# Performance work log

Hardware: AMD Instinct MI355X
Metric: run time of the kernel (lower is better)

The kernel has to match this reference:

```python
import jax, jax.numpy as jnp
import numpy as np

N_NODES = 50000
N_EDGES = 600000
HIDDEN = 128
HEADS = 4
HEAD_DIM = HIDDEN // HEADS
RBF = 40


def setup_inputs() -> dict:
    key = jax.random.key(0)
    ks = jax.random.split(key, 16)
    def lin(k, fan_in, fan_out):
        return jax.random.normal(k, (fan_in, fan_out), jnp.float32) / np.sqrt(fan_in)
    return {
        "x": jax.random.normal(ks[0], (N_NODES, HIDDEN), jnp.float32),
        "edge_index": jax.random.randint(ks[1], (2, N_EDGES), 0, N_NODES, jnp.int32),
        "edge_attr_rbf": jax.random.normal(ks[2], (N_EDGES, RBF), jnp.float32),
        "is_defect": jax.random.randint(ks[3], (N_NODES,), 0, 2, jnp.int32),
        "Wq": lin(ks[4], HIDDEN, HIDDEN), "bq": jnp.zeros((HIDDEN,), jnp.float32),
        "Wk": lin(ks[5], HIDDEN, HIDDEN), "bk": jnp.zeros((HIDDEN,), jnp.float32),
        "Wv": lin(ks[6], HIDDEN, HIDDEN), "bv": jnp.zeros((HIDDEN,), jnp.float32),
        "Wo": lin(ks[7], HIDDEN, HIDDEN), "bo": jnp.zeros((HIDDEN,), jnp.float32),
        "Wg1": lin(ks[8], RBF, HIDDEN), "bg1": jnp.zeros((HIDDEN,), jnp.float32),
        "Wg2": lin(ks[9], HIDDEN, HEADS), "bg2": jnp.zeros((HEADS,), jnp.float32),
        "defect_bias": jax.random.normal(ks[10], (HEADS, 4), jnp.float32),
    }


def reference(x, edge_index, edge_attr_rbf, is_defect,
              Wq, bq, Wk, bk, Wv, bv, Wo, bo, Wg1, bg1, Wg2, bg2, defect_bias):
    N = x.shape[0]
    Q = (x @ Wq + bq).reshape(N, HEADS, HEAD_DIM)
    K = (x @ Wk + bk).reshape(N, HEADS, HEAD_DIM)
    V = (x @ Wv + bv).reshape(N, HEADS, HEAD_DIM)
    src, dst = edge_index[0], edge_index[1]
    # per-edge attention scores [E, H]
    score = (Q[src] * K[dst]).sum(-1) / np.sqrt(HEAD_DIM)
    geo_bias = jax.nn.silu(edge_attr_rbf @ Wg1 + bg1) @ Wg2 + bg2  # [E, H]
    defect_code = is_defect[src] * 2 + is_defect[dst]  # [E] in {0,1,2,3}
    score = score + geo_bias + defect_bias[:, defect_code].T
    # segment softmax over edges grouped by dst
    smax = jax.ops.segment_max(score, dst, num_segments=N)  # [N, H]
    e = jnp.exp(score - smax[dst])
    denom = jax.ops.segment_sum(e, dst, num_segments=N)  # [N, H]
    alpha = e / denom[dst]
    msg = V[src] * alpha[..., None]  # [E, H, Hd]
    out = jax.ops.segment_sum(msg, dst, num_segments=N).reshape(N, HIDDEN)
    return out @ Wo + bo
```

## Files before the change

kernel.cpp:

```cpp
#include <hip/hip_runtime.h>
#include <math.h>

#define NN 50000
#define NE 600000
#define HID 128
#define NH 4
#define HD 32
#define NRBF 40
#define SCALE 0.17677669529663687f

typedef __attribute__((ext_vector_type(8))) __bf16 bf16x8;
typedef __attribute__((ext_vector_type(4))) __bf16 bf16x4;
typedef __attribute__((ext_vector_type(4))) float f32x4;

#define MFMA16(a, b, c) __builtin_amdgcn_mfma_f32_16x16x32_bf16(a, b, c, 0, 0, 0)

__device__ __forceinline__ void split2(float v, __bf16& h, __bf16& l) {
  h = (__bf16)v;
  l = (__bf16)(v - (float)h);
}

__global__ void k_prepw(const float* __restrict__ W, __bf16* __restrict__ hi,
                        __bf16* __restrict__ lo, int NKS, int KREAL) {
  int slot = blockIdx.x * 256 + threadIdx.x;
  int total = 8 * NKS * 4 * 16;
  if (slot >= total) return;
  int n = slot & 15, kg = (slot >> 4) & 3;
  int tt = slot >> 6;
  int ks = tt % NKS, nt = tt / NKS;
  bf16x8 h8, l8;
#pragma unroll
  for (int j = 0; j < 8; ++j) {
    int k = ks * 32 + kg * 8 + j;
    float v = (k < KREAL) ? W[k * 128 + nt * 16 + n] : 0.f;
    __bf16 h, l;
    split2(v, h, l);
    h8[j] = h;
    l8[j] = l;
  }
  *(bf16x8*)&hi[slot * 8] = h8;
  *(bf16x8*)&lo[slot * 8] = l8;
}

__global__ __launch_bounds__(256) void k_qkv3(
    const float* __restrict__ x,
    const __bf16* __restrict__ qhi, const __bf16* __restrict__ qlo,
    const __bf16* __restrict__ khi, const __bf16* __restrict__ klo,
    const __bf16* __restrict__ vhi, const __bf16* __restrict__ vlo,
    const float* __restrict__ bq, const float* __restrict__ bk,
    const float* __restrict__ bv,
    float* __restrict__ Q, float* __restrict__ K, float* __restrict__ V,
    int M) {
  __shared__ __bf16 Ahi[16384];
  __shared__ __bf16 Alo[16384];
  int t = threadIdx.x;
  int row0 = blockIdx.x * 128;

#pragma unroll
  for (int rep = 0; rep < 16; ++rep) {
    int idx = rep * 256 + t;
    int e = idx >> 5, c = idx & 31;
    int gn = row0 + e;
    float4 a = (gn < M) ? *(const float4*)&x[gn * 128 + c * 4]
                        : make_float4(0.f, 0.f, 0.f, 0.f);
    int mt = e >> 4, m = e & 15, ks = c >> 3, kg = (c >> 1) & 3, half = c & 1;
    int base = ((((mt * 4 + ks) * 4 + kg) * 16) + m) * 8 + half * 4;
    bf16x4 h4, l4;
    __bf16 h, l;
    split2(a.x, h, l); h4[0] = h; l4[0] = l;
    split2(a.y, h, l); h4[1] = h; l4[1] = l;
    split2(a.z, h, l); h4[2] = h; l4[2] = l;
    split2(a.w, h, l); h4[3] = h; l4[3] = l;
    *(bf16x4*)&Ahi[base] = h4;
    *(bf16x4*)&Alo[base] = l4;
  }
  __syncthreads();

  int wave = t >> 6, l = t & 63;
  int lq = l >> 4, ln = l & 15;
  int nt0 = wave * 2;
  const __bf16* whi[3] = {qhi, khi, vhi};
  const __bf16* wlo[3] = {qlo, klo, vlo};
  const float* bias[3] = {bq, bk, bv};
  float* out[3] = {Q, K, V};
  const f32x4 fz = {0.f, 0.f, 0.f, 0.f};

#pragma unroll
  for (int w = 0; w < 3; ++w) {
    bf16x8 Bh[2][4], Bl[2][4];
#pragma unroll
    for (int ntl = 0; ntl < 2; ++ntl)
#pragma unroll
      for (int ks = 0; ks < 4; ++ks) {
        int bidx = (((nt0 + ntl) * 4 + ks) * 4 + lq) * 16 + ln;
        Bh[ntl][ks] = *(const bf16x8*)&whi[w][bidx * 8];
        Bl[ntl][ks] = *(const bf16x8*)&wlo[w][bidx * 8];
      }
    f32x4 acc[8][2];
#pragma unroll
    for (int mt = 0; mt < 8; ++mt) { acc[mt][0] = fz; acc[mt][1] = fz; }
#pragma unroll
    for (int mt = 0; mt < 8; ++mt)
#pragma unroll
      for (int ks = 0; ks < 4; ++ks) {
        int as = ((((mt * 4 + ks) * 4 + lq) * 16) + ln) * 8;
        bf16x8 ah = *(bf16x8*)&Ahi[as];
        bf16x8 al = *(bf16x8*)&Alo[as];
#pragma unroll
        for (int ntl = 0; ntl < 2; ++ntl) {
          acc[mt][ntl] = MFMA16(ah, Bh[ntl][ks], acc[mt][ntl]);
          acc[mt][ntl] = MFMA16(al, Bh[ntl][ks], acc[mt][ntl]);
          acc[mt][ntl] = MFMA16(ah, Bl[ntl][ks], acc[mt][ntl]);
        }
      }
    int n0 = nt0 * 16 + ln;
    float b0 = bias[w][n0], b1 = bias[w][n0 + 16];
#pragma unroll
    for (int mt = 0; mt < 8; ++mt)
#pragma unroll
      for (int reg = 0; reg < 4; ++reg) {
        int e = row0 + mt * 16 + lq * 4 + reg;
        if (e < M) {
          out[w][e * 128 + n0] = acc[mt][0][reg] + b0;
          out[w][e * 128 + n0 + 16] = acc[mt][1][reg] + b1;
        }
      }
  }
}

__global__ __launch_bounds__(256) void k_mm128(
    const float* __restrict__ A, const __bf16* __restrict__ whi,
    const __bf16* __restrict__ wlo, const float* __restrict__ bias,
    float* __restrict__ out, int M) {
  __shared__ __bf16 Ahi[16384];
  __shared__ __bf16 Alo[16384];
  int t = threadIdx.x;
  int row0 = blockIdx.x * 128;
#pragma unroll
  for (int rep = 0; rep < 16; ++rep) {
    int idx = rep * 256 + t;
    int e = idx >> 5, c = idx & 31;
    int gn = row0 + e;
    float4 a = (gn < M) ? *(const float4*)&A[gn * 128 + c * 4]
                        : make_float4(0.f, 0.f, 0.f, 0.f);
    int mt = e >> 4, m = e & 15, ks = c >> 3, kg = (c >> 1) & 3, half = c & 1;
    int base = ((((mt * 4 + ks) * 4 + kg) * 16) + m) * 8 + half * 4;
    bf16x4 h4, l4;
    __bf16 h, l;
    split2(a.x, h, l); h4[0] = h; l4[0] = l;
    split2(a.y, h, l); h4[1] = h; l4[1] = l;
    split2(a.z, h, l); h4[2] = h; l4[2] = l;
    split2(a.w, h, l); h4[3] = h; l4[3] = l;
    *(bf16x4*)&Ahi[base] = h4;
    *(bf16x4*)&Alo[base] = l4;
  }
  __syncthreads();

  int wave = t >> 6, l = t & 63;
  int lq = l >> 4, ln = l & 15;
  int nt0 = wave * 2;
  const f32x4 fz = {0.f, 0.f, 0.f, 0.f};
  bf16x8 Bh[2][4], Bl[2][4];
#pragma unroll
  for (int ntl = 0; ntl < 2; ++ntl)
#pragma unroll
    for (int ks = 0; ks < 4; ++ks) {
      int bidx = (((nt0 + ntl) * 4 + ks) * 4 + lq) * 16 + ln;
      Bh[ntl][ks] = *(const bf16x8*)&whi[bidx * 8];
      Bl[ntl][ks] = *(const bf16x8*)&wlo[bidx * 8];
    }
  f32x4 acc[8][2];
#pragma unroll
  for (int mt = 0; mt < 8; ++mt) { acc[mt][0] = fz; acc[mt][1] = fz; }
#pragma unroll
  for (int mt = 0; mt < 8; ++mt)
#pragma unroll
    for (int ks = 0; ks < 4; ++ks) {
      int as = ((((mt * 4 + ks) * 4 + lq) * 16) + ln) * 8;
      bf16x8 ah = *(bf16x8*)&Ahi[as];
      bf16x8 al = *(bf16x8*)&Alo[as];
#pragma unroll
      for (int ntl = 0; ntl < 2; ++ntl) {
        acc[mt][ntl] = MFMA16(ah, Bh[ntl][ks], acc[mt][ntl]);
        acc[mt][ntl] = MFMA16(al, Bh[ntl][ks], acc[mt][ntl]);
        acc[mt][ntl] = MFMA16(ah, Bl[ntl][ks], acc[mt][ntl]);
      }
    }
  int n0 = nt0 * 16 + ln;
  float b0 = bias[n0], b1 = bias[n0 + 16];
#pragma unroll
  for (int mt = 0; mt < 8; ++mt)
#pragma unroll
    for (int reg = 0; reg < 4; ++reg) {
      int e = row0 + mt * 16 + lq * 4 + reg;
      if (e < M) {
        out[e * 128 + n0] = acc[mt][0][reg] + b0;
        out[e * 128 + n0 + 16] = acc[mt][1][reg] + b1;
      }
    }
}

__global__ __launch_bounds__(256) void k_geo_mfma(
    const float* __restrict__ rbf, const __bf16* __restrict__ g1hi,
    const __bf16* __restrict__ g1lo, const float* __restrict__ bg1,
    const float* __restrict__ Wg2, const float* __restrict__ bg2,
    const int* __restrict__ srcv, const int* __restrict__ dstv,
    const int* __restrict__ isd, const float* __restrict__ db,
    float* __restrict__ biasE) {
  __shared__ __bf16 Ahi[8192];
  __shared__ __bf16 Alo[8192];
  int t = threadIdx.x;
  int e0 = blockIdx.x * 128;

  bf16x8 zz = {};
#pragma unroll
  for (int z = 0; z < 4; ++z) {
    *(bf16x8*)&Ahi[(z * 256 + t) * 8] = zz;
    *(bf16x8*)&Alo[(z * 256 + t) * 8] = zz;
  }
  __syncthreads();
#pragma unroll
  for (int rep = 0; rep < 5; ++rep) {
    int idx = rep * 256 + t;
    int e = idx / 10, c = idx % 10;
    int ge = e0 + e;
    float4 a = (ge < NE) ? *(const float4*)&rbf[ge * NRBF + c * 4]
                         : make_float4(0.f, 0.f, 0.f, 0.f);
    int k4 = c * 4;
    int mt = e >> 4, m = e & 15, ks = k4 >> 5, kg = (k4 >> 3) & 3,
        half = (k4 >> 2) & 1;
    int base = ((((mt * 2 + ks) * 4 + kg) * 16) + m) * 8 + half * 4;
    bf16x4 h4, l4;
    __bf16 h, l;
    split2(a.x, h, l); h4[0] = h; l4[0] = l;
    split2(a.y, h, l); h4[1] = h; l4[1] = l;
    split2(a.z, h, l); h4[2] = h; l4[2] = l;
    split2(a.w, h, l); h4[3] = h; l4[3] = l;
    *(bf16x4*)&Ahi[base] = h4;
    *(bf16x4*)&Alo[base] = l4;
  }
  __syncthreads();

  int wave = t >> 6, l = t & 63;
  int lq = l >> 4, ln = l & 15;
  int mtb = wave * 2;
  const f32x4 fz = {0.f, 0.f, 0.f, 0.f};
  f32x4 acc[2][8];
#pragma unroll
  for (int mtl = 0; mtl < 2; ++mtl)
#pragma unroll
    for (int nt = 0; nt < 8; ++nt) acc[mtl][nt] = fz;

#pragma unroll
  for (int ks = 0; ks < 2; ++ks) {
    bf16x8 ah[2], al[2];
#pragma unroll
    for (int mtl = 0; mtl < 2; ++mtl) {
      int as = (((((mtb + mtl) * 2 + ks) * 4 + lq) * 16) + ln) * 8;
      ah[mtl] = *(bf16x8*)&Ahi[as];
      al[mtl] = *(bf16x8*)&Alo[as];
    }
#pragma unroll
    for (int nt = 0; nt < 8; ++nt) {
      int bidx = ((nt * 2 + ks) * 4 + lq) * 16 + ln;
      bf16x8 bh = *(const bf16x8*)&g1hi[bidx * 8];
      bf16x8 bl = *(const bf16x8*)&g1lo[bidx * 8];
#pragma unroll
      for (int mtl = 0; mtl < 2; ++mtl) {
        acc[mtl][nt] = MFMA16(ah[mtl], bh, acc[mtl][nt]);
        acc[mtl][nt] = MFMA16(al[mtl], bh, acc[mtl][nt]);
        acc[mtl][nt] = MFMA16(ah[mtl], bl, acc[mtl][nt]);
      }
    }
  }

  float p[2][4][4];
#pragma unroll
  for (int mtl = 0; mtl < 2; ++mtl)
#pragma unroll
    for (int reg = 0; reg < 4; ++reg)
#pragma unroll
      for (int hh = 0; hh < 4; ++hh) p[mtl][reg][hh] = 0.f;
#pragma unroll
  for (int nt = 0; nt < 8; ++nt) {
    int n = nt * 16 + ln;
    float b1v = bg1[n];
    float4 w2 = *(const float4*)&Wg2[n * 4];
#pragma unroll
    for (int mtl = 0; mtl < 2; ++mtl)
#pragma unroll
      for (int reg = 0; reg < 4; ++reg) {
        float h = acc[mtl][nt][reg] + b1v;
        float s = h / (1.f + __expf(-h));
        p[mtl][reg][0] = fmaf(s, w2.x, p[mtl][reg][0]);
        p[mtl][reg][1] = fmaf(s, w2.y, p[mtl][reg][1]);
        p[mtl][reg][2] = fmaf(s, w2.z, p[mtl][reg][2]);
        p[mtl][reg][3] = fmaf(s, w2.w, p[mtl][reg][3]);
      }
  }
#pragma unroll
  for (int off = 1; off < 16; off <<= 1)
#pragma unroll
    for (int mtl = 0; mtl < 2; ++mtl)
#pragma unroll
      for (int reg = 0; reg < 4; ++reg)
#pragma unroll
        for (int hh = 0; hh < 4; ++hh)
          p[mtl][reg][hh] += __shfl_xor(p[mtl][reg][hh], off, 64);
#pragma unroll
  for (int mtl = 0; mtl < 2; ++mtl) {
    float v = 0.f;
#pragma unroll
    for (int reg = 0; reg < 4; ++reg)
#pragma unroll
      for (int hh = 0; hh < 4; ++hh)
        if (ln == reg * 4 + hh) v = p[mtl][reg][hh];
    int reg = ln >> 2, hh = ln & 3;
    int e = e0 + (mtb + mtl) * 16 + lq * 4 + reg;
    if (e < NE) {
      int code = isd[srcv[e]] * 2 + isd[dstv[e]];
      biasE[e * 4 + hh] = v + bg2[hh] + db[hh * 4 + code];
    }
  }
}

__global__ void k_count(const int* __restrict__ dstv, int* __restrict__ cnt) {
  int e = blockIdx.x * 256 + threadIdx.x;
  if (e < NE) atomicAdd(&cnt[dstv[e]], 1);
}

__global__ void k_scan1(const int* __restrict__ cnt, int* __restrict__ bsum) {
  __shared__ int sd[256];
  int t = threadIdx.x;
  int i = blockIdx.x * 256 + t;
  sd[t] = (i < NN) ? cnt[i] : 0;
  __syncthreads();
  for (int off = 128; off > 0; off >>= 1) {
    if (t < off) sd[t] += sd[t + off];
    __syncthreads();
  }
  if (t == 0) bsum[blockIdx.x] = sd[0];
}

__global__ void k_scan2(const int* __restrict__ bsum, int* __restrict__ bpre,
                        int* __restrict__ offsets, int nb) {
  __shared__ int sd[256];
  int t = threadIdx.x;
  int v = (t < nb) ? bsum[t] : 0;
  sd[t] = v;
  __syncthreads();
  for (int off = 1; off < 256; off <<= 1) {
    int x = (t >= off) ? sd[t - off] : 0;
    __syncthreads();
    sd[t] += x;
    __syncthreads();
  }
  if (t < nb) bpre[t] = sd[t] - v;
  if (t == 255) offsets[NN] = sd[255];
}

__global__ void k_scan3(const int* __restrict__ cnt, const int* __restrict__ bpre,
                        int* __restrict__ offsets, int* __restrict__ cursor) {
  __shared__ int sd[256];
  int t = threadIdx.x;
  int i = blockIdx.x * 256 + t;
  int v = (i < NN) ? cnt[i] : 0;
  sd[t] = v;
  __syncthreads();
  for (int off = 1; off < 256; off <<= 1) {
    int x = (t >= off) ? sd[t - off] : 0;
    __syncthreads();
    sd[t] += x;
    __syncthreads();
  }
  int excl = sd[t] - v + bpre[blockIdx.x];
  if (i < NN) { offsets[i] = excl; cursor[i] = excl; }
}

__global__ void k_scatter(const int* __restrict__ srcv,
                          const int* __restrict__ dstv,
                          int* __restrict__ cursor,
                          int* __restrict__ eids, int* __restrict__ srcCSR) {
  int e = blockIdx.x * 256 + threadIdx.x;
  if (e < NE) {
    int d = dstv[e];
    int pos = atomicAdd(&cursor[d], 1);
    eids[pos] = e;
    srcCSR[pos] = srcv[e];
  }
}

__global__ __launch_bounds__(128) void k_agg_fused(
    const int* __restrict__ srcCSR, const int* __restrict__ eids,
    const int* __restrict__ offsets, const float* __restrict__ biasE,
    const float* __restrict__ Q, const float* __restrict__ K,
    const float* __restrict__ V, float* __restrict__ accum) {
  int b = blockIdx.x;
  int t = threadIdx.x;
  int h = t >> 5;
  int beg = offsets[b], end = offsets[b + 1];
  float kv = K[b * HID + t];

  float m = -3.0e38f, den = 0.f, acc = 0.f;
  int s_n = (beg < end) ? srcCSR[beg] : 0;
  int e_n = (beg < end) ? eids[beg] : 0;
  for (int i = beg; i < end; ++i) {
    int s = s_n, e = e_n;
    if (i + 1 < end) {
      s_n = srcCSR[i + 1];
      e_n = eids[i + 1];
    }
    float qv = Q[s * HID + t];
    float vv = V[s * HID + t];
    float bias = biasE[e * 4 + h];
    float prod = qv * kv;
#pragma unroll
    for (int off = 1; off < 32; off <<= 1)
      prod += __shfl_xor(prod, off, 32);
    float sc = fmaf(prod, SCALE, bias);
    float mn = fmaxf(m, sc);
    float r = __expf(m - mn);
    float w = __expf(sc - mn);
    den = fmaf(den, r, w);
    acc = fmaf(acc, r, w * vv);
    m = mn;
  }
  accum[b * HID + t] = (end > beg) ? (acc / den) : 0.f;
}

extern "C" void kernel_launch(void* const* d_in, const int* in_sizes, int n_in,
                              void* d_out, int out_size, void* d_ws, size_t ws_size,
                              hipStream_t stream) {
  const float* x = (const float*)d_in[0];
  const int* ei = (const int*)d_in[1];
  const float* rbf = (const float*)d_in[2];
  const int* isd = (const int*)d_in[3];
  const float* Wq = (const float*)d_in[4];
  const float* bq = (const float*)d_in[5];
  const float* Wk = (const float*)d_in[6];
  const float* bk = (const float*)d_in[7];
  const float* Wv = (const float*)d_in[8];
  const float* bv = (const float*)d_in[9];
  const float* Wo = (const float*)d_in[10];
  const float* bo = (const float*)d_in[11];
  const float* Wg1 = (const float*)d_in[12];
  const float* bg1 = (const float*)d_in[13];
  const float* Wg2 = (const float*)d_in[14];
  const float* bg2 = (const float*)d_in[15];
  const float* db = (const float*)d_in[16];
  const int* srcv = ei;
  const int* dstv = ei + NE;

  char* p = (char*)d_ws;
  auto alloc = [&](size_t bytes) {
    void* r = (void*)p;
    p += (bytes + 255) & ~(size_t)255;
    return r;
  };
  float* Q = (float*)alloc((size_t)NN * HID * 4);
  float* Kb = (float*)alloc((size_t)NN * HID * 4);
  float* Vb = (float*)alloc((size_t)NN * HID * 4);
  float* biasE = (float*)alloc((size_t)NE * NH * 4);
  float* accum = (float*)alloc((size_t)NN * HID * 4);
  int* cnt = (int*)alloc((size_t)NN * 4);
  int* offsets = (int*)alloc((size_t)(NN + 1) * 4);
  int* cursor = (int*)alloc((size_t)NN * 4);
  int* eids = (int*)alloc((size_t)NE * 4);
  int* srcCSR = (int*)alloc((size_t)NE * 4);
  int* bsum = (int*)alloc(256 * 4);
  int* bpre = (int*)alloc(256 * 4);
  __bf16* qhi = (__bf16*)alloc(2048 * 8 * 2);
  __bf16* qlo = (__bf16*)alloc(2048 * 8 * 2);
  __bf16* khi = (__bf16*)alloc(2048 * 8 * 2);
  __bf16* klo = (__bf16*)alloc(2048 * 8 * 2);
  __bf16* vhi = (__bf16*)alloc(2048 * 8 * 2);
  __bf16* vlo = (__bf16*)alloc(2048 * 8 * 2);
  __bf16* ohi = (__bf16*)alloc(2048 * 8 * 2);
  __bf16* olo = (__bf16*)alloc(2048 * 8 * 2);
  __bf16* g1hi = (__bf16*)alloc(1024 * 8 * 2);
  __bf16* g1lo = (__bf16*)alloc(1024 * 8 * 2);

  hipMemsetAsync(cnt, 0, (size_t)NN * 4, stream);

  int gQ = (NN + 127) / 128;
  int gE = (NE + 127) / 128;
  int gEth = (NE + 255) / 256;
  int gS = (NN + 255) / 256;

  k_prepw<<<8, 256, 0, stream>>>(Wq, qhi, qlo, 4, 128);
  k_prepw<<<8, 256, 0, stream>>>(Wk, khi, klo, 4, 128);
  k_prepw<<<8, 256, 0, stream>>>(Wv, vhi, vlo, 4, 128);
  k_prepw<<<8, 256, 0, stream>>>(Wo, ohi, olo, 4, 128);
  k_prepw<<<4, 256, 0, stream>>>(Wg1, g1hi, g1lo, 2, NRBF);

  k_qkv3<<<gQ, 256, 0, stream>>>(x, qhi, qlo, khi, klo, vhi, vlo,
                                 bq, bk, bv, Q, Kb, Vb, NN);
  k_geo_mfma<<<gE, 256, 0, stream>>>(rbf, g1hi, g1lo, bg1, Wg2, bg2,
                                     srcv, dstv, isd, db, biasE);
  k_count<<<gEth, 256, 0, stream>>>(dstv, cnt);
  k_scan1<<<gS, 256, 0, stream>>>(cnt, bsum);
  k_scan2<<<1, 256, 0, stream>>>(bsum, bpre, offsets, gS);
  k_scan3<<<gS, 256, 0, stream>>>(cnt, bpre, offsets, cursor);
  k_scatter<<<gEth, 256, 0, stream>>>(srcv, dstv, cursor, eids, srcCSR);
  k_agg_fused<<<NN, 128, 0, stream>>>(srcCSR, eids, offsets, biasE,
                                      Q, Kb, Vb, accum);
  k_mm128<<<gQ, 256, 0, stream>>>(accum, ohi, olo, bo, (float*)d_out, NN);
}
```

Before: 497.0 us.

## Store Q and V as bf16 and drop low-part split in geo GEMM

Q and V are now written in bf16 and read as bf16 in the per-destination aggregation kernel, halving the bytes gathered per edge. K stays fp32. The geo-bias GEMM no longer splits rbf into hi/lo parts, which removes one MFMA per tile and the matching LDS buffer. It also XOR-swizzles the LDS layout to reduce bank conflicts. The cost is lower precision in the scores, the messages and the geo bias, which could push results past the tolerance.

```diff
diff --git a/kernel.cpp b/kernel.cpp
--- a/kernel.cpp
+++ b/kernel.cpp
@@ -49,7 +49,7 @@
     const __bf16* __restrict__ vhi, const __bf16* __restrict__ vlo,
     const float* __restrict__ bq, const float* __restrict__ bk,
     const float* __restrict__ bv,
-    float* __restrict__ Q, float* __restrict__ K, float* __restrict__ V,
+    __bf16* __restrict__ Qb, float* __restrict__ K, __bf16* __restrict__ Vb,
     int M) {
   __shared__ __bf16 Ahi[16384];
   __shared__ __bf16 Alo[16384];
@@ -82,7 +82,6 @@
   const __bf16* whi[3] = {qhi, khi, vhi};
   const __bf16* wlo[3] = {qlo, klo, vlo};
   const float* bias[3] = {bq, bk, bv};
-  float* out[3] = {Q, K, V};
   const f32x4 fz = {0.f, 0.f, 0.f, 0.f};
 
 #pragma unroll
@@ -121,8 +120,16 @@
       for (int reg = 0; reg < 4; ++reg) {
         int e = row0 + mt * 16 + lq * 4 + reg;
         if (e < M) {
-          out[w][e * 128 + n0] = acc[mt][0][reg] + b0;
-          out[w][e * 128 + n0 + 16] = acc[mt][1][reg] + b1;
+          float v0 = acc[mt][0][reg] + b0;
+          float v1 = acc[mt][1][reg] + b1;
+          if (w == 1) {
+            K[e * 128 + n0] = v0;
+            K[e * 128 + n0 + 16] = v1;
+          } else {
+            __bf16* dst = (w == 0) ? Qb : Vb;
+            dst[e * 128 + n0] = (__bf16)v0;
+            dst[e * 128 + n0 + 16] = (__bf16)v1;
+          }
         }
       }
   }
@@ -208,16 +215,12 @@
     const int* __restrict__ isd, const float* __restrict__ db,
     float* __restrict__ biasE) {
   __shared__ __bf16 Ahi[8192];
-  __shared__ __bf16 Alo[8192];
   int t = threadIdx.x;
   int e0 = blockIdx.x * 128;
 
   bf16x8 zz = {};
 #pragma unroll
-  for (int z = 0; z < 4; ++z) {
-    *(bf16x8*)&Ahi[(z * 256 + t) * 8] = zz;
-    *(bf16x8*)&Alo[(z * 256 + t) * 8] = zz;
-  }
+  for (int z = 0; z < 4; ++z) *(bf16x8*)&Ahi[(z * 256 + t) * 8] = zz;
   __syncthreads();
 #pragma unroll
   for (int rep = 0; rep < 5; ++rep) {
@@ -229,15 +232,13 @@
     int k4 = c * 4;
     int mt = e >> 4, m = e & 15, ks = k4 >> 5, kg = (k4 >> 3) & 3,
         half = (k4 >> 2) & 1;
-    int base = ((((mt * 2 + ks) * 4 + kg) * 16) + m) * 8 + half * 4;
-    bf16x4 h4, l4;
-    __bf16 h, l;
-    split2(a.x, h, l); h4[0] = h; l4[0] = l;
-    split2(a.y, h, l); h4[1] = h; l4[1] = l;
-    split2(a.z, h, l); h4[2] = h; l4[2] = l;
-    split2(a.w, h, l); h4[3] = h; l4[3] = l;
+    int base = ((((mt * 2 + ks) * 4 + kg) * 16) + (m ^ kg)) * 8 + half * 4;
+    bf16x4 h4;
+    h4[0] = (__bf16)a.x;
+    h4[1] = (__bf16)a.y;
+    h4[2] = (__bf16)a.z;
+    h4[3] = (__bf16)a.w;
     *(bf16x4*)&Ahi[base] = h4;
-    *(bf16x4*)&Alo[base] = l4;
   }
   __syncthreads();
 
@@ -253,12 +254,11 @@
 
 #pragma unroll
   for (int ks = 0; ks < 2; ++ks) {
-    bf16x8 ah[2], al[2];
+    bf16x8 ah[2];
 #pragma unroll
     for (int mtl = 0; mtl < 2; ++mtl) {
-      int as = (((((mtb + mtl) * 2 + ks) * 4 + lq) * 16) + ln) * 8;
+      int as = (((((mtb + mtl) * 2 + ks) * 4 + lq) * 16) + (ln ^ lq)) * 8;
       ah[mtl] = *(bf16x8*)&Ahi[as];
-      al[mtl] = *(bf16x8*)&Alo[as];
     }
 #pragma unroll
     for (int nt = 0; nt < 8; ++nt) {
@@ -268,7 +268,6 @@
 #pragma unroll
       for (int mtl = 0; mtl < 2; ++mtl) {
         acc[mtl][nt] = MFMA16(ah[mtl], bh, acc[mtl][nt]);
-        acc[mtl][nt] = MFMA16(al[mtl], bh, acc[mtl][nt]);
         acc[mtl][nt] = MFMA16(ah[mtl], bl, acc[mtl][nt]);
       }
     }
@@ -393,8 +392,8 @@
 __global__ __launch_bounds__(128) void k_agg_fused(
     const int* __restrict__ srcCSR, const int* __restrict__ eids,
     const int* __restrict__ offsets, const float* __restrict__ biasE,
-    const float* __restrict__ Q, const float* __restrict__ K,
-    const float* __restrict__ V, float* __restrict__ accum) {
+    const __bf16* __restrict__ Qb, const float* __restrict__ K,
+    const __bf16* __restrict__ Vb, float* __restrict__ accum) {
   int b = blockIdx.x;
   int t = threadIdx.x;
   int h = t >> 5;
@@ -410,8 +409,8 @@
       s_n = srcCSR[i + 1];
       e_n = eids[i + 1];
     }
-    float qv = Q[s * HID + t];
-    float vv = V[s * HID + t];
+    float qv = (float)Qb[s * HID + t];
+    float vv = (float)Vb[s * HID + t];
     float bias = biasE[e * 4 + h];
     float prod = qv * kv;
 #pragma unroll
@@ -457,9 +456,9 @@
     p += (bytes + 255) & ~(size_t)255;
     return r;
   };
-  float* Q = (float*)alloc((size_t)NN * HID * 4);
+  __bf16* Qb = (__bf16*)alloc((size_t)NN * HID * 2);
   float* Kb = (float*)alloc((size_t)NN * HID * 4);
-  float* Vb = (float*)alloc((size_t)NN * HID * 4);
+  __bf16* Vb = (__bf16*)alloc((size_t)NN * HID * 2);
   float* biasE = (float*)alloc((size_t)NE * NH * 4);
   float* accum = (float*)alloc((size_t)NN * HID * 4);
   int* cnt = (int*)alloc((size_t)NN * 4);
@@ -494,7 +493,7 @@
   k_prepw<<<4, 256, 0, stream>>>(Wg1, g1hi, g1lo, 2, NRBF);
 
   k_qkv3<<<gQ, 256, 0, stream>>>(x, qhi, qlo, khi, klo, vhi, vlo,
-                                 bq, bk, bv, Q, Kb, Vb, NN);
+                                 bq, bk, bv, Qb, Kb, Vb, NN);
   k_geo_mfma<<<gE, 256, 0, stream>>>(rbf, g1hi, g1lo, bg1, Wg2, bg2,
                                      srcv, dstv, isd, db, biasE);
   k_count<<<gEth, 256, 0, stream>>>(dstv, cnt);
@@ -503,6 +502,6 @@
   k_scan3<<<gS, 256, 0, stream>>>(cnt, bpre, offsets, cursor);
   k_scatter<<<gEth, 256, 0, stream>>>(srcv, dstv, cursor, eids, srcCSR);
   k_agg_fused<<<NN, 128, 0, stream>>>(srcCSR, eids, offsets, biasE,
-                                      Q, Kb, Vb, accum);
+                                      Qb, Kb, Vb, accum);
   k_mm128<<<gQ, 256, 0, stream>>>(accum, ohi, olo, bo, (float*)d_out, NN);
 }
```

New measurement: 488.5 us. Within noise of the previous version (-1.7%).
